# Kernel optimization log

Measured on AMD Instinct MI355X. Metric: run time of the kernel, lower is better.

The kernel has to match this reference:

```python
import jax, jax.numpy as jnp
import numpy as np

IN_DIM, H, E_DIM = 32, 64, 16
N_NODES, N_EDGES = 50000, 100000


def setup_inputs() -> dict:
    key = jax.random.key(0)
    ks = jax.random.split(key, 12)
    x = jax.random.normal(ks[0], (N_NODES, IN_DIM), dtype=jnp.float32)
    edge_index = jax.random.randint(ks[1], (2, N_EDGES), 0, N_NODES, dtype=jnp.int64)
    edge_attr = jax.random.uniform(ks[2], (N_EDGES, E_DIM), dtype=jnp.float32)
    def lin(k, fan_in, shape):
        return jax.random.normal(k, shape, dtype=jnp.float32) / np.sqrt(fan_in)
    return {
        "x": x,
        "edge_index": edge_index,
        "edge_attr": edge_attr,
        # lin0: Linear(in_dim, h)
        "lin0_w": lin(ks[3], IN_DIM, (H, IN_DIM)),
        "lin0_b": jnp.zeros((H,), jnp.float32),
        # NNConv's edge network: Linear(edge_dim, h*h)
        "nn_w": lin(ks[4], E_DIM, (H * H, E_DIM)),
        "nn_b": jnp.zeros((H * H,), jnp.float32),
        # NNConv root weight [in_ch, out_ch] and bias
        "root": lin(ks[5], H, (H, H)),
        "conv_b": jnp.zeros((H,), jnp.float32),
        # GRU (single layer): weight_ih [3h,h], weight_hh [3h,h], biases [3h]
        "w_ih": lin(ks[6], H, (3 * H, H)),
        "w_hh": lin(ks[7], H, (3 * H, H)),
        "b_ih": jnp.zeros((3 * H,), jnp.float32),
        "b_hh": jnp.zeros((3 * H,), jnp.float32),
    }


def _nnconv(x, src, dst, edge_attr, nn_w, nn_b, root, conv_b, num_nodes):
    # per-edge weight matrices [E, h_in, h_out] from the edge MLP
    W_e = (edge_attr @ nn_w.T + nn_b).reshape(-1, H, H)
    # gather source features, per-edge matvec, scatter-add to destinations
    msg = jnp.einsum('ei,eio->eo', x[src], W_e)          # [E, h]
    agg = jax.ops.segment_sum(msg, dst, num_segments=num_nodes)
    return agg + x @ root + conv_b


def _gru_step(x, h, w_ih, w_hh, b_ih, b_hh):
    gi = x @ w_ih.T + b_ih                                # [N, 3h]
    gh = h @ w_hh.T + b_hh
    i_r, i_z, i_n = jnp.split(gi, 3, axis=-1)
    h_r, h_z, h_n = jnp.split(gh, 3, axis=-1)
    r = jax.nn.sigmoid(i_r + h_r)
    z = jax.nn.sigmoid(i_z + h_z)
    n = jnp.tanh(i_n + r * h_n)
    return (1.0 - z) * n + z * h


def reference(x, edge_index, edge_attr, lin0_w, lin0_b, nn_w, nn_b,
              root, conv_b, w_ih, w_hh, b_ih, b_hh):
    src, dst = edge_index[0], edge_index[1]
    num_nodes = x.shape[0]
    out = jax.nn.relu(x @ lin0_w.T + lin0_b)              # [N, h]
    h = out
    for _ in range(3):
        m = jax.nn.relu(_nnconv(out, src, dst, edge_attr, nn_w, nn_b,
                                root, conv_b, num_nodes))
        h = _gru_step(m, h, w_ih, w_hh, b_ih, b_hh)
        out = h
    return out
```

## Files before the change

### kernel.cpp

```cpp
#include <hip/hip_runtime.h>
#include <hip/hip_bf16.h>

typedef unsigned short u16;
typedef __attribute__((ext_vector_type(8))) _Float16 h8v;
typedef __attribute__((ext_vector_type(4))) float f32x4;

#define CAP 32

static __device__ __forceinline__ u16 f2h(float f) {
    _Float16 h = (_Float16)f;
    u16 r; __builtin_memcpy(&r, &h, 2); return r;
}
static __device__ __forceinline__ float h2f(u16 b) {
    _Float16 h; __builtin_memcpy(&h, &b, 2); return (float)h;
}
static __device__ __forceinline__ float sigm(float x) {
    return 1.f / (1.f + __expf(-x));
}
static __device__ __forceinline__ float tanh_f(float x) {
    return 1.f - 2.f / (__expf(2.f * x) + 1.f);
}

__global__ __launch_bounds__(256) void k_prep(
        const float* __restrict__ nn_w, const float* __restrict__ nn_b,
        const float* __restrict__ root, const float* __restrict__ w_hh,
        const float* __restrict__ w_ih, const float* __restrict__ lin0_w,
        const float* __restrict__ ea,
        u16* __restrict__ wf2, u16* __restrict__ w1, u16* __restrict__ w2,
        u16* __restrict__ w0, u16* __restrict__ ea16, int* __restrict__ deg,
        int N, int nEA) {
    int idx = blockIdx.x * 256 + threadIdx.x;
    if (idx < 34 * 4 * 512) {
        int j = idx & 7, lane = (idx >> 3) & 63;
        int rest = idx >> 9;
        int ct = rest & 3, kc = rest >> 2;
        int kappa = kc * 32 + ((lane >> 4) * 8) + j;
        int o = ct * 16 + (lane & 15);
        float v;
        if (kappa < 1024) {
            int k = kappa >> 6, i = kappa & 63;
            v = nn_w[(size_t)(i * 64 + o) * 16 + k];
        } else {
            v = nn_b[(size_t)(kappa - 1024) * 64 + o];
        }
        wf2[idx] = f2h(v);
    }
    if (idx < 16384 + 12288 + 2048) {
        if (idx < 16384) {
            int j = idx & 7, lane = (idx >> 3) & 63;
            int rest = idx >> 9;
            int ct = rest & 15, kc = rest >> 4;
            int k = kc * 32 + ((lane >> 4) * 8) + j;
            int col = ct * 16 + (lane & 15);
            float v = (col < 64) ? root[(size_t)k * 64 + col]
                                 : w_hh[(size_t)(col - 64) * 64 + k];
            w1[idx] = f2h(v);
        } else if (idx < 16384 + 12288) {
            int i2 = idx - 16384;
            int j = i2 & 7, lane = (i2 >> 3) & 63;
            int rest = i2 >> 9;
            int ct = rest % 12, kc = rest / 12;
            int k = kc * 32 + ((lane >> 4) * 8) + j;
            int col = ct * 16 + (lane & 15);
            w2[i2] = f2h(w_ih[(size_t)col * 64 + k]);
        } else {
            int i3 = idx - 16384 - 12288;
            int j = i3 & 7, lane = (i3 >> 3) & 63;
            int ct = i3 >> 9;
            int k = ((lane >> 4) * 8) + j;
            int col = ct * 16 + (lane & 15);
            w0[i3] = f2h(lin0_w[(size_t)col * 32 + k]);
        }
    }
    if (idx < N) deg[idx] = 0;
    if (idx < nEA) ea16[idx] = f2h(ea[idx]);
}

__global__ __launch_bounds__(256) void k_build(
        const int* __restrict__ ei, int* __restrict__ deg,
        int* __restrict__ tab, int E) {
    int e = blockIdx.x * 256 + threadIdx.x;
    if (e < E) {
        int dst = ei[E + e];
        int pos = atomicAdd(&deg[dst], 1);
        if (pos < CAP) tab[(size_t)dst * CAP + pos] = e;
    }
}

__global__ __launch_bounds__(256) void k_lin0(
        const float* __restrict__ x, const u16* __restrict__ w0,
        const float* __restrict__ b, float* __restrict__ out, int N) {
    int t = threadIdx.x, l = t & 63, w = t >> 6, g = l >> 4;
    int n0 = blockIdx.x * 64 + w * 16;
    int node = n0 + (l & 15);
    int nc = node < N ? node : N - 1;
    const float* xrow = x + (size_t)nc * 32 + g * 8;
    float4 xa = *(const float4*)(xrow);
    float4 xb = *(const float4*)(xrow + 4);
    h8v xh;
    xh[0] = (_Float16)xa.x; xh[1] = (_Float16)xa.y;
    xh[2] = (_Float16)xa.z; xh[3] = (_Float16)xa.w;
    xh[4] = (_Float16)xb.x; xh[5] = (_Float16)xb.y;
    xh[6] = (_Float16)xb.z; xh[7] = (_Float16)xb.w;

    f32x4 acc[4];
    #pragma unroll
    for (int ct = 0; ct < 4; ct++) {
        h8v wh = *(const h8v*)((const _Float16*)w0 + (ct * 64 + l) * 8);
        acc[ct] = __builtin_amdgcn_mfma_f32_16x16x32_f16(wh, xh, (f32x4)(0.f), 0, 0, 0);
    }
    if (node < N) {
        #pragma unroll
        for (int ct = 0; ct < 4; ct++) {
            int c = ct * 16 + g * 4;
            f32x4 bb = *(const f32x4*)(b + c);
            f32x4 ov;
            #pragma unroll
            for (int r = 0; r < 4; r++) ov[r] = fmaxf(acc[ct][r] + bb[r], 0.f);
            *(f32x4*)(out + (size_t)node * 64 + c) = ov;
        }
    }
}

__global__ __launch_bounds__(256) void k_AB(
        const float* __restrict__ x, const u16* __restrict__ ea16,
        const u16* __restrict__ wf2, const int* __restrict__ ei,
        u16* __restrict__ msg, int E) {
    __shared__ __align__(16) u16 Ab[64 * 512];
    int t = threadIdx.x, l = t & 63, w = t >> 6, g = l >> 4;
    int ctH = blockIdx.y;
    int eblk = blockIdx.x * 256 + w * 64;

    int eact[4];
    h8v xf0[4], xf1[4], eav[4][2];
    #pragma unroll
    for (int et = 0; et < 4; et++) {
        int e = eblk + et * 16 + (l & 15);
        eact[et] = e;
        int ec = e < E ? e : E - 1;
        int src = ei[ec];
        const float* xr = x + (size_t)src * 64 + g * 8;
        float4 v0 = *(const float4*)(xr);
        float4 v1 = *(const float4*)(xr + 4);
        float4 v2 = *(const float4*)(xr + 32);
        float4 v3 = *(const float4*)(xr + 36);
        h8v a, b;
        a[0] = (_Float16)v0.x; a[1] = (_Float16)v0.y;
        a[2] = (_Float16)v0.z; a[3] = (_Float16)v0.w;
        a[4] = (_Float16)v1.x; a[5] = (_Float16)v1.y;
        a[6] = (_Float16)v1.z; a[7] = (_Float16)v1.w;
        b[0] = (_Float16)v2.x; b[1] = (_Float16)v2.y;
        b[2] = (_Float16)v2.z; b[3] = (_Float16)v2.w;
        b[4] = (_Float16)v3.x; b[5] = (_Float16)v3.y;
        b[6] = (_Float16)v3.z; b[7] = (_Float16)v3.w;
        xf0[et] = a;
        xf1[et] = b;
        const _Float16* ep = (const _Float16*)ea16 + (size_t)ec * 16;
        eav[et][0] = *(const h8v*)(ep);
        eav[et][1] = *(const h8v*)(ep + 8);
    }

    const uint4* wf2u = (const uint4*)wf2;
    uint4* Abu = (uint4*)Ab;
    #pragma unroll
    for (int i = 0; i < 16; i++) {
        int j = i * 256 + t;
        int f = j >> 6, win = j & 63;
        int gf = (f >> 1) * 4 + ctH * 2 + (f & 1);
        Abu[j] = wf2u[(size_t)gf * 64 + win];
    }
    __syncthreads();

    f32x4 acc[4][2];
    #pragma unroll
    for (int et = 0; et < 4; et++)
        #pragma unroll
        for (int ct = 0; ct < 2; ct++) acc[et][ct] = (f32x4)(0.f);

    const _Float16* AbH = (const _Float16*)Ab;
    const _Float16* wfh = (const _Float16*)wf2;

    #pragma unroll
    for (int p = 0; p < 8; p++) {
        #pragma unroll
        for (int kcl = 0; kcl < 4; kcl++) {
            int kc = p * 4 + kcl;
            h8v af[2];
            #pragma unroll
            for (int ct = 0; ct < 2; ct++)
                af[ct] = *(const h8v*)(AbH + (size_t)(kc * 2 + ct) * 512 + l * 8);
            const int k = 2 * p + (kcl >> 1);
            #pragma unroll
            for (int et = 0; et < 4; et++) {
                _Float16 s = eav[et][k >> 3][k & 7];
                h8v es = {s, s, s, s, s, s, s, s};
                h8v zf = es * ((kcl & 1) ? xf1[et] : xf0[et]);
                #pragma unroll
                for (int ct = 0; ct < 2; ct++)
                    acc[et][ct] = __builtin_amdgcn_mfma_f32_16x16x32_f16(af[ct], zf, acc[et][ct], 0, 0, 0);
            }
        }
    }
    #pragma unroll
    for (int kcl = 0; kcl < 2; kcl++) {
        int kc = 32 + kcl;
        h8v af[2];
        #pragma unroll
        for (int ct = 0; ct < 2; ct++)
            af[ct] = *(const h8v*)(wfh + (size_t)(kc * 4 + ctH * 2 + ct) * 512 + l * 8);
        #pragma unroll
        for (int et = 0; et < 4; et++) {
            h8v zf = (kcl & 1) ? xf1[et] : xf0[et];
            #pragma unroll
            for (int ct = 0; ct < 2; ct++)
                acc[et][ct] = __builtin_amdgcn_mfma_f32_16x16x32_f16(af[ct], zf, acc[et][ct], 0, 0, 0);
        }
    }

    #pragma unroll
    for (int et = 0; et < 4; et++) {
        int e = eact[et];
        if (e < E) {
            u16* mr = msg + (size_t)e * 64 + g * 4;
            #pragma unroll
            for (int ct = 0; ct < 2; ct++) {
                ushort4 pk;
                pk.x = f2h(acc[et][ct][0]);
                pk.y = f2h(acc[et][ct][1]);
                pk.z = f2h(acc[et][ct][2]);
                pk.w = f2h(acc[et][ct][3]);
                *(ushort4*)(mr + (ctH * 2 + ct) * 16) = pk;
            }
        }
    }
}

__global__ __launch_bounds__(256) void k_C(
        const float* __restrict__ x, const u16* __restrict__ msg,
        const int* __restrict__ deg, const int* __restrict__ tab,
        const u16* __restrict__ w1, const u16* __restrict__ w2,
        const float* __restrict__ conv_b, const float* __restrict__ b_hh,
        const float* __restrict__ b_ih, float* __restrict__ hout, int N) {
    __shared__ float mld[4][16][68];
    int t = threadIdx.x, l = t & 63, w = t >> 6, g = l >> 4;
    int n0 = blockIdx.x * 64 + w * 16;
    int node = n0 + (l & 15);
    int nc = node < N ? node : N - 1;
    const float* xrow = x + (size_t)nc * 64 + g * 8;
    const _Float16* w1h = (const _Float16*)w1;
    const _Float16* w2h = (const _Float16*)w2;

    h8v xh[2];
    #pragma unroll
    for (int kc = 0; kc < 2; kc++) {
        f32x4 a = *(const f32x4*)(xrow + kc * 32);
        f32x4 b = *(const f32x4*)(xrow + kc * 32 + 4);
        #pragma unroll
        for (int j = 0; j < 8; j++) xh[kc][j] = (_Float16)(j < 4 ? a[j] : b[j - 4]);
    }

    f32x4 avs[4];
    #pragma unroll
    for (int ct = 0; ct < 4; ct++) avs[ct] = (f32x4)(0.f);
    if (node < N) {
        int dg = deg[node];
        dg = dg < CAP ? dg : CAP;
        const int* tr = tab + (size_t)node * CAP;
        for (int j = 0; j < dg; j++) {
            int eid = tr[j];
            const u16* mr = msg + (size_t)eid * 64 + g * 4;
            #pragma unroll
            for (int ct = 0; ct < 4; ct++) {
                ushort4 mv = *(const ushort4*)(mr + ct * 16);
                avs[ct][0] += h2f(mv.x);
                avs[ct][1] += h2f(mv.y);
                avs[ct][2] += h2f(mv.z);
                avs[ct][3] += h2f(mv.w);
            }
        }
    }

    f32x4 acc1[16];
    #pragma unroll
    for (int ct = 0; ct < 16; ct++) acc1[ct] = (f32x4)(0.f);
    #pragma unroll
    for (int kc = 0; kc < 2; kc++) {
        #pragma unroll
        for (int ct = 0; ct < 16; ct++) {
            h8v wh = *(const h8v*)(w1h + (size_t)(kc * 16 + ct) * 512 + l * 8);
            acc1[ct] = __builtin_amdgcn_mfma_f32_16x16x32_f16(wh, xh[kc], acc1[ct], 0, 0, 0);
        }
    }

    #pragma unroll
    for (int ct = 0; ct < 4; ct++) {
        int c = ct * 16 + g * 4;
        f32x4 cb = *(const f32x4*)(conv_b + c);
        f32x4 mv;
        #pragma unroll
        for (int r = 0; r < 4; r++) mv[r] = fmaxf(acc1[ct][r] + avs[ct][r] + cb[r], 0.f);
        *(f32x4*)(&mld[w][l & 15][c]) = mv;
    }
    #pragma unroll
    for (int ct = 4; ct < 16; ct++) {
        int c = (ct - 4) * 16 + g * 4;
        f32x4 bh = *(const f32x4*)(b_hh + c);
        #pragma unroll
        for (int r = 0; r < 4; r++) acc1[ct][r] += bh[r];
    }
    __syncthreads();

    h8v mh[2];
    #pragma unroll
    for (int kc = 0; kc < 2; kc++) {
        const float* mr = &mld[w][l & 15][kc * 32 + g * 8];
        f32x4 a = *(const f32x4*)(mr);
        f32x4 b = *(const f32x4*)(mr + 4);
        #pragma unroll
        for (int j = 0; j < 8; j++) mh[kc][j] = (_Float16)(j < 4 ? a[j] : b[j - 4]);
    }

    f32x4 acc2[12];
    #pragma unroll
    for (int ct = 0; ct < 12; ct++) acc2[ct] = (f32x4)(0.f);
    #pragma unroll
    for (int kc = 0; kc < 2; kc++) {
        #pragma unroll
        for (int ct = 0; ct < 12; ct++) {
            h8v wh = *(const h8v*)(w2h + (size_t)(kc * 12 + ct) * 512 + l * 8);
            acc2[ct] = __builtin_amdgcn_mfma_f32_16x16x32_f16(wh, mh[kc], acc2[ct], 0, 0, 0);
        }
    }

    #pragma unroll
    for (int q = 0; q < 4; q++) {
        int c = q * 16 + g * 4;
        f32x4 bir = *(const f32x4*)(b_ih + c);
        f32x4 biz = *(const f32x4*)(b_ih + 64 + c);
        f32x4 bin = *(const f32x4*)(b_ih + 128 + c);
        f32x4 hv = (f32x4)(0.f);
        if (node < N) hv = *(const f32x4*)(x + (size_t)node * 64 + c);
        f32x4 outv;
        #pragma unroll
        for (int r = 0; r < 4; r++) {
            float rr = sigm(acc2[q][r] + bir[r] + acc1[4 + q][r]);
            float zz = sigm(acc2[4 + q][r] + biz[r] + acc1[8 + q][r]);
            float nt = tanh_f(acc2[8 + q][r] + bin[r] + rr * acc1[12 + q][r]);
            outv[r] = (1.f - zz) * nt + zz * hv[r];
        }
        if (node < N) *(f32x4*)(hout + (size_t)node * 64 + c) = outv;
    }
}

extern "C" void kernel_launch(void* const* d_in, const int* in_sizes, int n_in,
                              void* d_out, int out_size, void* d_ws, size_t ws_size,
                              hipStream_t stream) {
    const float* x_in   = (const float*)d_in[0];
    const int*   ei     = (const int*)d_in[1];
    const float* ea     = (const float*)d_in[2];
    const float* lin0_w = (const float*)d_in[3];
    const float* lin0_b = (const float*)d_in[4];
    const float* nn_w   = (const float*)d_in[5];
    const float* nn_b   = (const float*)d_in[6];
    const float* root   = (const float*)d_in[7];
    const float* conv_b = (const float*)d_in[8];
    const float* w_ih   = (const float*)d_in[9];
    const float* w_hh   = (const float*)d_in[10];
    const float* b_ih   = (const float*)d_in[11];
    const float* b_hh   = (const float*)d_in[12];

    int N = in_sizes[0] / 32;
    int E = in_sizes[1] / 2;

    char* ws = (char*)d_ws;
    size_t off = 0;
    auto alloc = [&](size_t bytes) { char* p = ws + off; off += (bytes + 255) & ~(size_t)255; return p; };
    float* xbuf   = (float*)alloc((size_t)N * 64 * 4);
    u16*   msg    = (u16*)alloc((size_t)E * 64 * 2);
    u16*   wf2    = (u16*)alloc((size_t)34 * 4 * 512 * 2);
    u16*   ea16   = (u16*)alloc((size_t)E * 16 * 2);
    u16*   w1     = (u16*)alloc(16384 * 2);
    u16*   w2     = (u16*)alloc(12288 * 2);
    u16*   w0     = (u16*)alloc(2048 * 2);
    int*   deg    = (int*)alloc((size_t)N * 4);
    int*   tab    = (int*)alloc((size_t)N * CAP * 4);
    (void)ws_size;

    int nEA = E * 16;
    hipLaunchKernelGGL(k_prep, dim3((nEA + 255) / 256), dim3(256), 0, stream,
                       nn_w, nn_b, root, w_hh, w_ih, lin0_w, ea,
                       wf2, w1, w2, w0, ea16, deg, N, nEA);
    hipLaunchKernelGGL(k_build, dim3((E + 255) / 256), dim3(256), 0, stream, ei, deg, tab, E);
    hipLaunchKernelGGL(k_lin0, dim3((N + 63) / 64), dim3(256), 0, stream, x_in, w0, lin0_b, xbuf, N);

    for (int it = 0; it < 3; it++) {
        hipLaunchKernelGGL(k_AB, dim3((E + 255) / 256, 2), dim3(256), 0, stream,
                           xbuf, ea16, wf2, ei, msg, E);
        float* hout = (it == 2) ? (float*)d_out : xbuf;
        hipLaunchKernelGGL(k_C, dim3((N + 63) / 64), dim3(256), 0, stream, xbuf, msg,
                           deg, tab, w1, w2, conv_b, b_hh, b_ih, hout, N);
    }
}
```

Baseline: 173.8 us.

## Merge edge-table build with lin0 launch and stage w1 weights in LDS

Merges the CSR-style destination table build and the initial lin0 projection into one launch, using a block-index split, to save one kernel launch and its gap. In k_C, the 32 KB w1 weight matrix is now copied cooperatively into shared memory before the MFMA loop, instead of every wave reading it from global/L2. The copy adds a 32 KB LDS footprint per block and a barrier, which can reduce occupancy and delay the start of the MFMA work.

```diff
diff --git a/kernel.cpp b/kernel.cpp
--- a/kernel.cpp
+++ b/kernel.cpp
@@ -76,25 +76,29 @@
     if (idx < nEA) ea16[idx] = f2h(ea[idx]);
 }
 
-__global__ __launch_bounds__(256) void k_build(
-        const int* __restrict__ ei, int* __restrict__ deg,
-        int* __restrict__ tab, int E) {
-    int e = blockIdx.x * 256 + threadIdx.x;
-    if (e < E) {
-        int dst = ei[E + e];
-        int pos = atomicAdd(&deg[dst], 1);
-        if (pos < CAP) tab[(size_t)dst * CAP + pos] = e;
-    }
-}
-
-__global__ __launch_bounds__(256) void k_lin0(
-        const float* __restrict__ x, const u16* __restrict__ w0,
-        const float* __restrict__ b, float* __restrict__ out, int N) {
-    int t = threadIdx.x, l = t & 63, w = t >> 6, g = l >> 4;
-    int n0 = blockIdx.x * 64 + w * 16;
+__global__ __launch_bounds__(256) void k_pre2(
+        const int* __restrict__ ei, int* __restrict__ deg, int* __restrict__ tab,
+        const float* __restrict__ x_in, const u16* __restrict__ w0,
+        const float* __restrict__ lin0_b, float* __restrict__ x0,
+        int N, int E) {
+    int nbuild = (E + 255) / 256;
+    int bid = blockIdx.x;
+    int t = threadIdx.x;
+    if (bid < nbuild) {
+        int e = bid * 256 + t;
+        if (e < E) {
+            int dst = ei[E + e];
+            int pos = atomicAdd(&deg[dst], 1);
+            if (pos < CAP) tab[(size_t)dst * CAP + pos] = e;
+        }
+        return;
+    }
+    int b2 = bid - nbuild;
+    int l = t & 63, w = t >> 6, g = l >> 4;
+    int n0 = b2 * 64 + w * 16;
     int node = n0 + (l & 15);
     int nc = node < N ? node : N - 1;
-    const float* xrow = x + (size_t)nc * 32 + g * 8;
+    const float* xrow = x_in + (size_t)nc * 32 + g * 8;
     float4 xa = *(const float4*)(xrow);
     float4 xb = *(const float4*)(xrow + 4);
     h8v xh;
@@ -102,7 +106,6 @@
     xh[2] = (_Float16)xa.z; xh[3] = (_Float16)xa.w;
     xh[4] = (_Float16)xb.x; xh[5] = (_Float16)xb.y;
     xh[6] = (_Float16)xb.z; xh[7] = (_Float16)xb.w;
-
     f32x4 acc[4];
     #pragma unroll
     for (int ct = 0; ct < 4; ct++) {
@@ -113,11 +116,11 @@
         #pragma unroll
         for (int ct = 0; ct < 4; ct++) {
             int c = ct * 16 + g * 4;
-            f32x4 bb = *(const f32x4*)(b + c);
+            f32x4 bb = *(const f32x4*)(lin0_b + c);
             f32x4 ov;
             #pragma unroll
             for (int r = 0; r < 4; r++) ov[r] = fmaxf(acc[ct][r] + bb[r], 0.f);
-            *(f32x4*)(out + (size_t)node * 64 + c) = ov;
+            *(f32x4*)(x0 + (size_t)node * 64 + c) = ov;
         }
     }
 }
@@ -241,13 +244,13 @@
         const u16* __restrict__ w1, const u16* __restrict__ w2,
         const float* __restrict__ conv_b, const float* __restrict__ b_hh,
         const float* __restrict__ b_ih, float* __restrict__ hout, int N) {
+    __shared__ __align__(16) u16 w1s[16384];
     __shared__ float mld[4][16][68];
     int t = threadIdx.x, l = t & 63, w = t >> 6, g = l >> 4;
     int n0 = blockIdx.x * 64 + w * 16;
     int node = n0 + (l & 15);
     int nc = node < N ? node : N - 1;
     const float* xrow = x + (size_t)nc * 64 + g * 8;
-    const _Float16* w1h = (const _Float16*)w1;
     const _Float16* w2h = (const _Float16*)w2;
 
     h8v xh[2];
@@ -280,6 +283,15 @@
         }
     }
 
+    {
+        const uint4* w1u = (const uint4*)w1;
+        uint4* w1su = (uint4*)w1s;
+        #pragma unroll
+        for (int i = 0; i < 8; i++) w1su[i * 256 + t] = w1u[i * 256 + t];
+    }
+    __syncthreads();
+
+    const _Float16* w1sh = (const _Float16*)w1s;
     f32x4 acc1[16];
     #pragma unroll
     for (int ct = 0; ct < 16; ct++) acc1[ct] = (f32x4)(0.f);
@@ -287,7 +299,7 @@
     for (int kc = 0; kc < 2; kc++) {
         #pragma unroll
         for (int ct = 0; ct < 16; ct++) {
-            h8v wh = *(const h8v*)(w1h + (size_t)(kc * 16 + ct) * 512 + l * 8);
+            h8v wh = *(const h8v*)(w1sh + (size_t)(kc * 16 + ct) * 512 + l * 8);
             acc1[ct] = __builtin_amdgcn_mfma_f32_16x16x32_f16(wh, xh[kc], acc1[ct], 0, 0, 0);
         }
     }
@@ -387,17 +399,20 @@
     (void)ws_size;
 
     int nEA = E * 16;
+    int nbuild = (E + 255) / 256;
+    int ntile  = (N + 63) / 64;
+
     hipLaunchKernelGGL(k_prep, dim3((nEA + 255) / 256), dim3(256), 0, stream,
                        nn_w, nn_b, root, w_hh, w_ih, lin0_w, ea,
                        wf2, w1, w2, w0, ea16, deg, N, nEA);
-    hipLaunchKernelGGL(k_build, dim3((E + 255) / 256), dim3(256), 0, stream, ei, deg, tab, E);
-    hipLaunchKernelGGL(k_lin0, dim3((N + 63) / 64), dim3(256), 0, stream, x_in, w0, lin0_b, xbuf, N);
+    hipLaunchKernelGGL(k_pre2, dim3(nbuild + ntile), dim3(256), 0, stream,
+                       ei, deg, tab, x_in, w0, lin0_b, xbuf, N, E);
 
     for (int it = 0; it < 3; it++) {
         hipLaunchKernelGGL(k_AB, dim3((E + 255) / 256, 2), dim3(256), 0, stream,
                            xbuf, ea16, wf2, ei, msg, E);
         float* hout = (it == 2) ? (float*)d_out : xbuf;
-        hipLaunchKernelGGL(k_C, dim3((N + 63) / 64), dim3(256), 0, stream, xbuf, msg,
+        hipLaunchKernelGGL(k_C, dim3(ntile), dim3(256), 0, stream, xbuf, msg,
                            deg, tab, w1, w2, conv_b, b_hh, b_ih, hout, N);
     }
 }
```

Result: slower. 189.4 us (+9.0%).
